# Optimization experiments

Hardware: AMD Instinct MI355X
Metric: run time of the kernel (lower is better)

## Reference

```python
import jax, jax.numpy as jnp
import numpy as np

TEMPERATURE = 5.656854249492381  # sqrt(d_k)=sqrt(32)


def setup_inputs() -> dict:
    key = jax.random.key(0)
    k1, k2, k3, k4 = jax.random.split(key, 4)
    B, L, H, DK, DV = 4, 1024, 8, 32, 32
    q = jax.random.normal(k1, (B, L, H * DK), dtype=jnp.float32)
    k = jax.random.normal(k2, (B, L, H * DK), dtype=jnp.float32)
    v = jax.random.normal(k3, (B, L, H * DV), dtype=jnp.float32)
    a_k = jax.random.normal(k4, (L, L, DK), dtype=jnp.float32)
    return {"q": q, "k": k, "v": v, "a_k": a_k, "d_k": DK, "d_v": DV, "n_head": H}


def reference(q, k, v, a_k, d_k, d_v, n_head):
    B, Lq, _ = q.shape
    Lv = v.shape[1]
    # [B, H, L, d]
    rq = q.reshape(B, Lq, n_head, d_k).transpose(0, 2, 1, 3)
    rk = k.reshape(B, Lq, n_head, d_k).transpose(0, 2, 1, 3)
    rv = v.reshape(B, Lv, n_head, d_v).transpose(0, 2, 1, 3)
    # attn[b,h,i,j] = sum_d rq[b,h,j,d] * rk[b,h,i,d] * a_k[i,j,d]
    # (dim 2 indexes k positions, dim 3 indexes q positions, per the torch broadcast)
    attn = jnp.einsum('bhjd,bhid,ijd->bhij', rq, rk, a_k) / TEMPERATURE
    attn = jax.nn.softmax(attn, axis=-1)
    # dropout is identity in eval mode
    out = jnp.einsum('bhij,bhjd->bhid', attn, rv)
    return out, attn
```

## Files before the change

kernel.cpp:

```cpp
#include <hip/hip_runtime.h>
#include <cstddef>

#define B_  4
#define L_  1024
#define H_  8
#define DK_ 32
#define DV_ 32
#define BH_ 32
#define HD_ 256

#define INV_T 0.17677669529663687f

__global__ __launch_bounds__(256) void transpose_q(
    const float* __restrict__ q, float* __restrict__ qT)
{
    const int bh  = blockIdx.x >> 2;
    const int jt  = blockIdx.x & 3;
    const int b   = bh >> 3, h = bh & 7;
    const int tid = threadIdx.x;

    __shared__ float t_s[256][33];

    const float* qb = q + (size_t)b * L_ * HD_ + h * DK_;
    #pragma unroll
    for (int rep = 0; rep < 8; ++rep) {
        const int f = rep * 1024 + tid * 4;
        const int j = f >> 5, d = f & 31;
        float4 val = *reinterpret_cast<const float4*>(qb + (size_t)(jt * 256 + j) * HD_ + d);
        t_s[j][d + 0] = val.x; t_s[j][d + 1] = val.y;
        t_s[j][d + 2] = val.z; t_s[j][d + 3] = val.w;
    }
    __syncthreads();
    float* qo = qT + (size_t)bh * (DK_ * L_) + jt * 256;
    #pragma unroll
    for (int d = 0; d < 32; ++d)
        qo[(size_t)d * L_ + tid] = t_s[tid][d];
}

__global__ __launch_bounds__(256) void score_kernel(
    const float* __restrict__ qT,
    const float* __restrict__ k,
    const float* __restrict__ a_k,
    float* __restrict__ attn_u,
    float* __restrict__ sums)
{
    const int bidx  = blockIdx.x;
    const int jhalf = bidx & 1;
    const int half  = (bidx >> 1) & 1;
    const int ig    = bidx >> 2;
    const int i0    = ig * 4;
    const int bh0   = half * 16;
    const int tid   = threadIdx.x;
    const int w     = __builtin_amdgcn_readfirstlane(tid >> 6);
    const int lane  = tid & 63;

    __shared__ float a_s[4][64][36];

    float rs[4][4] = {{0.f}};

    for (int jt = jhalf * 8; jt < jhalf * 8 + 8; ++jt) {
        const int j0 = jt * 64;
        __syncthreads();
        #pragma unroll
        for (int rep = 0; rep < 8; ++rep) {
            const int f  = rep * 1024 + tid * 4;
            const int ii = f >> 11, jj = (f >> 5) & 63, d = f & 31;
            float4 val = *reinterpret_cast<const float4*>(
                a_k + (size_t)(i0 + ii) * (L_ * DK_) + (size_t)(j0 + jj) * DK_ + d);
            *reinterpret_cast<float4*>(&a_s[ii][jj][d]) = val;
        }
        __syncthreads();

        float s[4][4];
        #pragma unroll
        for (int bhl = 0; bhl < 4; ++bhl)
            #pragma unroll
            for (int ii = 0; ii < 4; ++ii) s[bhl][ii] = 0.f;

        #pragma unroll 2
        for (int d4 = 0; d4 < 8; ++d4) {
            float4 av[4];
            #pragma unroll
            for (int ii = 0; ii < 4; ++ii)
                av[ii] = *reinterpret_cast<const float4*>(&a_s[ii][lane][d4 * 4]);
            #pragma unroll
            for (int bhl = 0; bhl < 4; ++bhl) {
                const int bh = bh0 + w * 4 + bhl;
                const int b  = bh >> 3, h = bh & 7;
                const float* qp = qT + (size_t)bh * (DK_ * L_) + (size_t)(d4 * 4) * L_ + j0 + lane;
                const float q0 = qp[0];
                const float q1 = qp[L_];
                const float q2 = qp[2 * L_];
                const float q3 = qp[3 * L_];
                const float* kp = k + (size_t)b * L_ * HD_ + (size_t)i0 * HD_ + h * DK_ + d4 * 4;
                #pragma unroll
                for (int ii = 0; ii < 4; ++ii) {
                    float4 kv = *reinterpret_cast<const float4*>(kp + ii * HD_);
                    s[bhl][ii] = fmaf(kv.x * av[ii].x, q0, s[bhl][ii]);
                    s[bhl][ii] = fmaf(kv.y * av[ii].y, q1, s[bhl][ii]);
                    s[bhl][ii] = fmaf(kv.z * av[ii].z, q2, s[bhl][ii]);
                    s[bhl][ii] = fmaf(kv.w * av[ii].w, q3, s[bhl][ii]);
                }
            }
        }

        #pragma unroll
        for (int bhl = 0; bhl < 4; ++bhl) {
            const int bh = bh0 + w * 4 + bhl;
            #pragma unroll
            for (int ii = 0; ii < 4; ++ii) {
                const float u = __expf(s[bhl][ii] * INV_T);
                rs[bhl][ii] += u;
                attn_u[((size_t)bh * L_ + (i0 + ii)) * L_ + j0 + lane] = u;
            }
        }
    }

    #pragma unroll
    for (int bhl = 0; bhl < 4; ++bhl) {
        #pragma unroll
        for (int ii = 0; ii < 4; ++ii) {
            float vsum = rs[bhl][ii];
            #pragma unroll
            for (int off = 32; off > 0; off >>= 1) vsum += __shfl_xor(vsum, off);
            if (lane == 0)
                sums[((size_t)jhalf * BH_ + bh0 + w * 4 + bhl) * L_ + i0 + ii] = vsum;
        }
    }
}

__global__ __launch_bounds__(256) void pv_kernel(
    const float* __restrict__ v,
    const float* __restrict__ sums,
    float* __restrict__ attn,
    float* __restrict__ out)
{
    const int bh  = blockIdx.x >> 6;
    const int ic  = blockIdx.x & 63;
    const int i0  = ic * 16;
    const int b   = bh >> 3, h = bh & 7;
    const int tid = threadIdx.x;
    const int r   = tid >> 4;
    const int t16 = tid & 15;

    __shared__ float v_s[64][36];
    __shared__ float u_s[16][68];

    const float inv = 1.0f / (sums[(size_t)bh * L_ + i0 + r] +
                              sums[(size_t)(BH_ + bh) * L_ + i0 + r]);
    float* arow = attn + ((size_t)bh * L_ + i0 + r) * L_;

    float a0 = 0.f, a1 = 0.f;

    for (int jt = 0; jt < 16; ++jt) {
        const int j0 = jt * 64;
        __syncthreads();
        {
            const int jj = tid >> 2, dv = (tid & 3) * 8;
            const float* vp = v + (size_t)b * L_ * HD_ + (size_t)(j0 + jj) * HD_ + h * DV_ + dv;
            float4 v0 = *reinterpret_cast<const float4*>(vp);
            float4 v1 = *reinterpret_cast<const float4*>(vp + 4);
            *reinterpret_cast<float4*>(&v_s[jj][dv])     = v0;
            *reinterpret_cast<float4*>(&v_s[jj][dv + 4]) = v1;
        }
        {
            float4 u0 = *reinterpret_cast<const float4*>(arow + j0 + t16 * 4);
            u0.x *= inv; u0.y *= inv; u0.z *= inv; u0.w *= inv;
            *reinterpret_cast<float4*>(&u_s[r][t16 * 4]) = u0;
            *reinterpret_cast<float4*>(arow + j0 + t16 * 4) = u0;
        }
        __syncthreads();
        #pragma unroll
        for (int jj = 0; jj < 64; ++jj) {
            const float ub = u_s[r][jj];
            const float2 vv = *reinterpret_cast<const float2*>(&v_s[jj][t16 * 2]);
            a0 = fmaf(ub, vv.x, a0);
            a1 = fmaf(ub, vv.y, a1);
        }
    }
    *reinterpret_cast<float2*>(out + ((size_t)bh * L_ + i0 + r) * DV_ + t16 * 2)
        = make_float2(a0, a1);
}

extern "C" void kernel_launch(void* const* d_in, const int* in_sizes, int n_in,
                              void* d_out, int out_size, void* d_ws, size_t ws_size,
                              hipStream_t stream) {
    const float* q   = (const float*)d_in[0];
    const float* k   = (const float*)d_in[1];
    const float* v   = (const float*)d_in[2];
    const float* a_k = (const float*)d_in[3];

    float* out  = (float*)d_out;
    float* attn = out + (size_t)BH_ * L_ * DV_;

    float* ws   = (float*)d_ws;
    float* sums = ws;
    float* qT   = ws + 2 * BH_ * L_;

    transpose_q<<<dim3(128),   dim3(256), 0, stream>>>(q, qT);
    score_kernel<<<dim3(1024), dim3(256), 0, stream>>>(qT, k, a_k, attn, sums);
    pv_kernel<<<dim3(2048),    dim3(256), 0, stream>>>(v, sums, attn, out);
}
```

Measured before the change: 411.3 us.

## Register-prefetch next tiles in score and PV kernels; interleave qT layout

Score and PV kernels now load the next a_k / attn+v tile into registers while computing on the current shared-memory tile, then commit it to shared memory after a barrier. The point is to hide global-load latency behind compute. qT is stored in a d4-interleaved layout so each lane reads q as a single float4 instead of four strided scalars. The PV kernel also handles 32 rows per block with float4 accumulators, halving the grid and widening the LDS reads. The cost is more registers, which may lower occupancy, plus an extra barrier per iteration.

```diff
diff --git a/kernel.cpp b/kernel.cpp
--- a/kernel.cpp
+++ b/kernel.cpp
@@ -31,10 +31,14 @@
         t_s[j][d + 2] = val.z; t_s[j][d + 3] = val.w;
     }
     __syncthreads();
-    float* qo = qT + (size_t)bh * (DK_ * L_) + jt * 256;
-    #pragma unroll
-    for (int d = 0; d < 32; ++d)
-        qo[(size_t)d * L_ + tid] = t_s[tid][d];
+    float* qo = qT + (size_t)bh * (DK_ * L_);
+    const int j = jt * 256 + tid;
+    #pragma unroll
+    for (int d4 = 0; d4 < 8; ++d4) {
+        float4 w = make_float4(t_s[tid][d4 * 4 + 0], t_s[tid][d4 * 4 + 1],
+                               t_s[tid][d4 * 4 + 2], t_s[tid][d4 * 4 + 3]);
+        *reinterpret_cast<float4*>(qo + (size_t)d4 * (L_ * 4) + (size_t)j * 4) = w;
+    }
 }
 
 __global__ __launch_bounds__(256) void score_kernel(
@@ -57,19 +61,38 @@
     __shared__ float a_s[4][64][36];
 
     float rs[4][4] = {{0.f}};
-
-    for (int jt = jhalf * 8; jt < jhalf * 8 + 8; ++jt) {
-        const int j0 = jt * 64;
-        __syncthreads();
-        #pragma unroll
-        for (int rep = 0; rep < 8; ++rep) {
-            const int f  = rep * 1024 + tid * 4;
-            const int ii = f >> 11, jj = (f >> 5) & 63, d = f & 31;
-            float4 val = *reinterpret_cast<const float4*>(
-                a_k + (size_t)(i0 + ii) * (L_ * DK_) + (size_t)(j0 + jj) * DK_ + d);
-            *reinterpret_cast<float4*>(&a_s[ii][jj][d]) = val;
-        }
-        __syncthreads();
+    float4 st[8];
+
+    const int jt0 = jhalf * 8, jtE = jt0 + 8;
+
+    #pragma unroll
+    for (int rep = 0; rep < 8; ++rep) {
+        const int f  = rep * 1024 + tid * 4;
+        const int ii = f >> 11, jj = (f >> 5) & 63, d = f & 31;
+        st[rep] = *reinterpret_cast<const float4*>(
+            a_k + (size_t)(i0 + ii) * (L_ * DK_) + (size_t)(jt0 * 64 + jj) * DK_ + d);
+    }
+    #pragma unroll
+    for (int rep = 0; rep < 8; ++rep) {
+        const int f  = rep * 1024 + tid * 4;
+        const int ii = f >> 11, jj = (f >> 5) & 63, d = f & 31;
+        *reinterpret_cast<float4*>(&a_s[ii][jj][d]) = st[rep];
+    }
+    __syncthreads();
+
+    for (int jt = jt0; jt < jtE; ++jt) {
+        const int j0   = jt * 64;
+        const bool more = (jt != jtE - 1);
+
+        if (more) {
+            #pragma unroll
+            for (int rep = 0; rep < 8; ++rep) {
+                const int f  = rep * 1024 + tid * 4;
+                const int ii = f >> 11, jj = (f >> 5) & 63, d = f & 31;
+                st[rep] = *reinterpret_cast<const float4*>(
+                    a_k + (size_t)(i0 + ii) * (L_ * DK_) + (size_t)(j0 + 64 + jj) * DK_ + d);
+            }
+        }
 
         float s[4][4];
         #pragma unroll
@@ -87,19 +110,16 @@
             for (int bhl = 0; bhl < 4; ++bhl) {
                 const int bh = bh0 + w * 4 + bhl;
                 const int b  = bh >> 3, h = bh & 7;
-                const float* qp = qT + (size_t)bh * (DK_ * L_) + (size_t)(d4 * 4) * L_ + j0 + lane;
-                const float q0 = qp[0];
-                const float q1 = qp[L_];
-                const float q2 = qp[2 * L_];
-                const float q3 = qp[3 * L_];
+                const float4 q4 = *reinterpret_cast<const float4*>(
+                    qT + (size_t)bh * (DK_ * L_) + (size_t)d4 * (L_ * 4) + (size_t)(j0 + lane) * 4);
                 const float* kp = k + (size_t)b * L_ * HD_ + (size_t)i0 * HD_ + h * DK_ + d4 * 4;
                 #pragma unroll
                 for (int ii = 0; ii < 4; ++ii) {
                     float4 kv = *reinterpret_cast<const float4*>(kp + ii * HD_);
-                    s[bhl][ii] = fmaf(kv.x * av[ii].x, q0, s[bhl][ii]);
-                    s[bhl][ii] = fmaf(kv.y * av[ii].y, q1, s[bhl][ii]);
-                    s[bhl][ii] = fmaf(kv.z * av[ii].z, q2, s[bhl][ii]);
-                    s[bhl][ii] = fmaf(kv.w * av[ii].w, q3, s[bhl][ii]);
+                    s[bhl][ii] = fmaf(kv.x * av[ii].x, q4.x, s[bhl][ii]);
+                    s[bhl][ii] = fmaf(kv.y * av[ii].y, q4.y, s[bhl][ii]);
+                    s[bhl][ii] = fmaf(kv.z * av[ii].z, q4.z, s[bhl][ii]);
+                    s[bhl][ii] = fmaf(kv.w * av[ii].w, q4.w, s[bhl][ii]);
                 }
             }
         }
@@ -114,6 +134,17 @@
                 attn_u[((size_t)bh * L_ + (i0 + ii)) * L_ + j0 + lane] = u;
             }
         }
+
+        __syncthreads();
+        if (more) {
+            #pragma unroll
+            for (int rep = 0; rep < 8; ++rep) {
+                const int f  = rep * 1024 + tid * 4;
+                const int ii = f >> 11, jj = (f >> 5) & 63, d = f & 31;
+                *reinterpret_cast<float4*>(&a_s[ii][jj][d]) = st[rep];
+            }
+        }
+        __syncthreads();
     }
 
     #pragma unroll
@@ -135,51 +166,79 @@
     float* __restrict__ attn,
     float* __restrict__ out)
 {
-    const int bh  = blockIdx.x >> 6;
-    const int ic  = blockIdx.x & 63;
-    const int i0  = ic * 16;
+    const int bh  = blockIdx.x >> 5;
+    const int ic  = blockIdx.x & 31;
+    const int i0  = ic * 32;
     const int b   = bh >> 3, h = bh & 7;
     const int tid = threadIdx.x;
-    const int r   = tid >> 4;
-    const int t16 = tid & 15;
+    const int r   = tid >> 3;
+    const int t8  = tid & 7;
+    const int dv0 = t8 * 4;
+    const int c8  = t8 * 8;
+    const int jv  = tid >> 2;
+    const int dvs = (tid & 3) * 8;
 
     __shared__ float v_s[64][36];
-    __shared__ float u_s[16][68];
+    __shared__ float u_s[32][68];
 
     const float inv = 1.0f / (sums[(size_t)bh * L_ + i0 + r] +
                               sums[(size_t)(BH_ + bh) * L_ + i0 + r]);
     float* arow = attn + ((size_t)bh * L_ + i0 + r) * L_;
-
-    float a0 = 0.f, a1 = 0.f;
+    const float* vbase = v + (size_t)b * L_ * HD_ + h * DV_;
+
+    float4 acc = make_float4(0.f, 0.f, 0.f, 0.f);
+
+    float4 u0, u1, v0, v1;
+    u0 = *reinterpret_cast<const float4*>(arow + c8);
+    u1 = *reinterpret_cast<const float4*>(arow + c8 + 4);
+    v0 = *reinterpret_cast<const float4*>(vbase + (size_t)jv * HD_ + dvs);
+    v1 = *reinterpret_cast<const float4*>(vbase + (size_t)jv * HD_ + dvs + 4);
+    u0.x *= inv; u0.y *= inv; u0.z *= inv; u0.w *= inv;
+    u1.x *= inv; u1.y *= inv; u1.z *= inv; u1.w *= inv;
+    *reinterpret_cast<float4*>(&u_s[r][c8])     = u0;
+    *reinterpret_cast<float4*>(&u_s[r][c8 + 4]) = u1;
+    *reinterpret_cast<float4*>(arow + c8)       = u0;
+    *reinterpret_cast<float4*>(arow + c8 + 4)   = u1;
+    *reinterpret_cast<float4*>(&v_s[jv][dvs])     = v0;
+    *reinterpret_cast<float4*>(&v_s[jv][dvs + 4]) = v1;
+    __syncthreads();
 
     for (int jt = 0; jt < 16; ++jt) {
         const int j0 = jt * 64;
-        __syncthreads();
-        {
-            const int jj = tid >> 2, dv = (tid & 3) * 8;
-            const float* vp = v + (size_t)b * L_ * HD_ + (size_t)(j0 + jj) * HD_ + h * DV_ + dv;
-            float4 v0 = *reinterpret_cast<const float4*>(vp);
-            float4 v1 = *reinterpret_cast<const float4*>(vp + 4);
-            *reinterpret_cast<float4*>(&v_s[jj][dv])     = v0;
-            *reinterpret_cast<float4*>(&v_s[jj][dv + 4]) = v1;
-        }
-        {
-            float4 u0 = *reinterpret_cast<const float4*>(arow + j0 + t16 * 4);
-            u0.x *= inv; u0.y *= inv; u0.z *= inv; u0.w *= inv;
-            *reinterpret_cast<float4*>(&u_s[r][t16 * 4]) = u0;
-            *reinterpret_cast<float4*>(arow + j0 + t16 * 4) = u0;
-        }
-        __syncthreads();
+        const bool more = (jt != 15);
+
+        if (more) {
+            u0 = *reinterpret_cast<const float4*>(arow + j0 + 64 + c8);
+            u1 = *reinterpret_cast<const float4*>(arow + j0 + 64 + c8 + 4);
+            v0 = *reinterpret_cast<const float4*>(vbase + (size_t)(j0 + 64 + jv) * HD_ + dvs);
+            v1 = *reinterpret_cast<const float4*>(vbase + (size_t)(j0 + 64 + jv) * HD_ + dvs + 4);
+        }
+
         #pragma unroll
         for (int jj = 0; jj < 64; ++jj) {
             const float ub = u_s[r][jj];
-            const float2 vv = *reinterpret_cast<const float2*>(&v_s[jj][t16 * 2]);
-            a0 = fmaf(ub, vv.x, a0);
-            a1 = fmaf(ub, vv.y, a1);
-        }
-    }
-    *reinterpret_cast<float2*>(out + ((size_t)bh * L_ + i0 + r) * DV_ + t16 * 2)
-        = make_float2(a0, a1);
+            const float4 vv = *reinterpret_cast<const float4*>(&v_s[jj][dv0]);
+            acc.x = fmaf(ub, vv.x, acc.x);
+            acc.y = fmaf(ub, vv.y, acc.y);
+            acc.z = fmaf(ub, vv.z, acc.z);
+            acc.w = fmaf(ub, vv.w, acc.w);
+        }
+
+        __syncthreads();
+        if (more) {
+            u0.x *= inv; u0.y *= inv; u0.z *= inv; u0.w *= inv;
+            u1.x *= inv; u1.y *= inv; u1.z *= inv; u1.w *= inv;
+            *reinterpret_cast<float4*>(&u_s[r][c8])     = u0;
+            *reinterpret_cast<float4*>(&u_s[r][c8 + 4]) = u1;
+            *reinterpret_cast<float4*>(arow + j0 + 64 + c8)     = u0;
+            *reinterpret_cast<float4*>(arow + j0 + 64 + c8 + 4) = u1;
+            *reinterpret_cast<float4*>(&v_s[jv][dvs])     = v0;
+            *reinterpret_cast<float4*>(&v_s[jv][dvs + 4]) = v1;
+        }
+        __syncthreads();
+    }
+
+    *reinterpret_cast<float4*>(out + ((size_t)bh * L_ + i0 + r) * DV_ + dv0) = acc;
 }
 
 extern "C" void kernel_launch(void* const* d_in, const int* in_sizes, int n_in,
@@ -199,5 +258,5 @@
 
     transpose_q<<<dim3(128),   dim3(256), 0, stream>>>(q, qT);
     score_kernel<<<dim3(1024), dim3(256), 0, stream>>>(qT, k, a_k, attn, sums);
-    pv_kernel<<<dim3(2048),    dim3(256), 0, stream>>>(v, sums, attn, out);
-}
+    pv_kernel<<<dim3(1024),    dim3(256), 0, stream>>>(v, sums, attn, out);
+}
```

Result: slower. 521.3 us (+26.7%).
